# Optimization experiments

Measured on AMD Instinct MI355X. Metric: run time of the kernel, lower is better.

The kernel has to match this reference:

```python
import jax, jax.numpy as jnp
import numpy as np

HIDDEN = 4096
N_HEADS = 32
N_KV_HEADS = 8
HEAD_DIM = HIDDEN // N_HEADS  # 128
N_GROUPS = N_HEADS // N_KV_HEADS  # 4
ROPE_THETA = 10000.0
NEG_INF = -1e9


def fake_quant(x):
    """Symmetric per-tensor int8 fake quantization (quantize -> dequantize)."""
    scale = jnp.maximum(jnp.max(jnp.abs(x)) / 127.0, 1e-8)
    return jnp.clip(jnp.round(x / scale), -127.0, 127.0) * scale


def q_linear(x, W):
    # torch Linear: y = x @ W.T ; both operands fake-quantized (dequant-inline GEMM)
    return jnp.einsum('bsh,oh->bso', fake_quant(x), fake_quant(W))


def rope_cos_sin(position_ids, head_dim, dtype):
    inv_freq = 1.0 / (ROPE_THETA ** (jnp.arange(0, head_dim, 2, dtype=jnp.float32) / head_dim))
    freqs = position_ids.astype(jnp.float32)[..., None] * inv_freq  # [b, s, hd/2]
    emb = jnp.concatenate([freqs, freqs], axis=-1)                   # [b, s, hd]
    return jnp.cos(emb).astype(dtype), jnp.sin(emb).astype(dtype)


def rotate_half(x):
    x1, x2 = jnp.split(x, 2, axis=-1)
    return jnp.concatenate([-x2, x1], axis=-1)


def setup_inputs() -> dict:
    key = jax.random.key(0)
    ks = jax.random.split(key, 6)
    b, s = 2, 1024
    hidden_states = jax.random.normal(ks[0], (b, s, HIDDEN), dtype=jnp.float32)
    # additive causal mask [b, 1, q, kv]
    causal = jnp.where(jnp.tril(jnp.ones((s, s), dtype=bool)), 0.0, NEG_INF).astype(jnp.float32)
    attention_mask = jnp.broadcast_to(causal[None, None], (b, 1, s, s))
    position_ids = jnp.broadcast_to(jnp.arange(s, dtype=jnp.int64)[None, :], (b, s))
    winit = 1.0 / np.sqrt(HIDDEN)
    Wq = jax.random.normal(ks[1], (HIDDEN, HIDDEN), dtype=jnp.float32) * winit
    Wk = jax.random.normal(ks[2], (N_KV_HEADS * HEAD_DIM, HIDDEN), dtype=jnp.float32) * winit
    Wv = jax.random.normal(ks[3], (N_KV_HEADS * HEAD_DIM, HIDDEN), dtype=jnp.float32) * winit
    Wo = jax.random.normal(ks[4], (HIDDEN, HIDDEN), dtype=jnp.float32) * winit
    return {"hidden_states": hidden_states, "attention_mask": attention_mask,
            "position_ids": position_ids, "Wq": Wq, "Wk": Wk, "Wv": Wv, "Wo": Wo}


def reference(hidden_states, attention_mask, position_ids, Wq, Wk, Wv, Wo):
    b, s, _ = hidden_states.shape
    dtype = hidden_states.dtype

    # quantized QKV projections
    q = q_linear(hidden_states, Wq).reshape(b, s, N_HEADS, HEAD_DIM).transpose(0, 2, 1, 3)
    k = q_linear(hidden_states, Wk).reshape(b, s, N_KV_HEADS, HEAD_DIM).transpose(0, 2, 1, 3)
    v = q_linear(hidden_states, Wv).reshape(b, s, N_KV_HEADS, HEAD_DIM).transpose(0, 2, 1, 3)

    # RoPE
    cos, sin = rope_cos_sin(position_ids, HEAD_DIM, dtype)  # [b, s, hd]
    cos, sin = cos[:, None], sin[:, None]                   # broadcast over heads
    q = q * cos + rotate_half(q) * sin
    k = k * cos + rotate_half(k) * sin

    # GQA: repeat kv heads
    k = jnp.repeat(k, N_GROUPS, axis=1)  # [b, H, s, hd]
    v = jnp.repeat(v, N_GROUPS, axis=1)

    # quantized QK^T (per-tensor fake quant on both operands)
    attn = jnp.einsum('bhqd,bhkd->bhqk', fake_quant(q), fake_quant(k)) / jnp.sqrt(
        jnp.asarray(HEAD_DIM, dtype=jnp.float32)).astype(dtype)
    attn = attn + attention_mask
    attn = jax.nn.softmax(attn.astype(jnp.float32), axis=-1).astype(dtype)
    # attention_dropout = 0.0 (inference)

    # quantized AV matmul
    out = jnp.einsum('bhqk,bhkd->bhqd', fake_quant(attn), fake_quant(v))
    out = out.transpose(0, 2, 1, 3).reshape(b, s, HIDDEN)
    out = q_linear(out, Wo)
    return out
```

## Files before the change

kernel.cpp:

```cpp
#include <hip/hip_runtime.h>
#include <math.h>

#define B_ 2
#define S_ 1024
#define HID 4096
#define NH 32
#define NKV 8
#define HD 128
#define LOG2E 1.44269504088896340736f

typedef short s16x8 __attribute__((ext_vector_type(8)));
typedef float f32x4 __attribute__((ext_vector_type(4)));
typedef int i32x4 __attribute__((ext_vector_type(4)));
typedef unsigned short u16;
typedef unsigned uint4v __attribute__((ext_vector_type(4)));
typedef signed char s8;

__device__ __forceinline__ i32x4 mfma_i8(i32x4 a, i32x4 b, i32x4 c) {
  return __builtin_amdgcn_mfma_i32_16x16x64_i8(a, b, c, 0, 0, 0);
}
__device__ __forceinline__ float get_scale(const unsigned* sc, int slot) {
  return fmaxf(__uint_as_float(sc[slot]) / 127.0f, 1e-8f);
}
__device__ __forceinline__ int q127(float x, float s) {
  return (int)fminf(fmaxf(rintf(x / s), -127.f), 127.f);
}
__device__ __forceinline__ unsigned pack4(float4 v, float s) {
  return (q127(v.x, s) & 255) | ((q127(v.y, s) & 255) << 8) |
         ((q127(v.z, s) & 255) << 16) | ((q127(v.w, s) & 255) << 24);
}
__device__ __forceinline__ float max4(float4 v) {
  return fmaxf(fmaxf(fabsf(v.x), fabsf(v.y)), fmaxf(fabsf(v.z), fabsf(v.w)));
}
__device__ __forceinline__ void gload16(const void* g, void* l) {
  __builtin_amdgcn_global_load_lds(
      (const __attribute__((address_space(1))) unsigned*)g,
      (__attribute__((address_space(3))) unsigned*)l, 16, 0, 0);
}
__device__ __forceinline__ void atomic_absmax(unsigned* out, float m, int lane) {
  #pragma unroll
  for (int o = 32; o >= 1; o >>= 1) m = fmaxf(m, __shfl_xor(m, o));
  if (lane == 0) atomicMax(out, __float_as_uint(m));
}

#define SB_() __builtin_amdgcn_sched_barrier(0)
#define PBAR() do { SB_(); __builtin_amdgcn_s_barrier(); SB_(); } while (0)
#define VM6() do { SB_(); asm volatile("s_waitcnt vmcnt(6)" ::: "memory"); } while (0)
#define VM0() do { SB_(); asm volatile("s_waitcnt vmcnt(0)" ::: "memory"); } while (0)

__device__ __forceinline__ void tensor_pick(int blk, int& r, int& b0, int& nb) {
  if (blk < 342)       { r = 0; b0 = 0;    nb = 342; }
  else if (blk < 1024) { r = 1; b0 = 342;  nb = 682; }
  else if (blk < 1195) { r = 2; b0 = 1024; nb = 171; }
  else if (blk < 1366) { r = 3; b0 = 1195; nb = 171; }
  else                 { r = 4; b0 = 1366; nb = 682; }
}

__global__ void absmax5_k(const float4* __restrict__ p0, const float4* __restrict__ p1,
                          const float4* __restrict__ p2, const float4* __restrict__ p3,
                          const float4* __restrict__ p4, unsigned* __restrict__ sc) {
  int r, b0, nb;
  tensor_pick(blockIdx.x, r, b0, nb);
  const float4* x; int n4;
  if (r == 0)      { x = p0; n4 = B_ * S_ * HID / 4; }
  else if (r == 1) { x = p1; n4 = HID * HID / 4; }
  else if (r == 2) { x = p2; n4 = NKV * HD * HID / 4; }
  else if (r == 3) { x = p3; n4 = NKV * HD * HID / 4; }
  else             { x = p4; n4 = HID * HID / 4; }
  const int ng = n4 >> 2;
  const int stride = nb * 256;
  float m0 = 0.f, m1 = 0.f, m2 = 0.f, m3 = 0.f;
  for (int g = (blockIdx.x - b0) * 256 + threadIdx.x; g < ng; g += stride) {
    const float4* p = x + g * 4;
    float4 v0 = p[0], v1 = p[1], v2 = p[2], v3 = p[3];
    m0 = fmaxf(m0, max4(v0)); m1 = fmaxf(m1, max4(v1));
    m2 = fmaxf(m2, max4(v2)); m3 = fmaxf(m3, max4(v3));
  }
  float m = fmaxf(fmaxf(m0, m1), fmaxf(m2, m3));
  atomic_absmax(sc + r, m, threadIdx.x & 63);
}

__global__ void quant5_k(const float4* __restrict__ p0, const float4* __restrict__ p1,
                         const float4* __restrict__ p2, const float4* __restrict__ p3,
                         const float4* __restrict__ p4,
                         unsigned* __restrict__ y0, unsigned* __restrict__ y1,
                         unsigned* __restrict__ y2, unsigned* __restrict__ y3,
                         unsigned* __restrict__ y4, const unsigned* __restrict__ sc) {
  int r, b0, nb;
  tensor_pick(blockIdx.x, r, b0, nb);
  const float4* x; unsigned* y; int n4;
  if (r == 0)      { x = p0; y = y0; n4 = B_ * S_ * HID / 4; }
  else if (r == 1) { x = p1; y = y1; n4 = HID * HID / 4; }
  else if (r == 2) { x = p2; y = y2; n4 = NKV * HD * HID / 4; }
  else if (r == 3) { x = p3; y = y3; n4 = NKV * HD * HID / 4; }
  else             { x = p4; y = y4; n4 = HID * HID / 4; }
  float s = get_scale(sc, r);
  const int ng = n4 >> 2;
  const int stride = nb * 256;
  for (int g = (blockIdx.x - b0) * 256 + threadIdx.x; g < ng; g += stride) {
    const float4* p = x + g * 4;
    float4 v0 = p[0], v1 = p[1], v2 = p[2], v3 = p[3];
    uint4v o;
    o[0] = pack4(v0, s); o[1] = pack4(v1, s);
    o[2] = pack4(v2, s); o[3] = pack4(v3, s);
    *(uint4v*)(y + g * 4) = o;
  }
}

__global__ void quant_k(const float4* __restrict__ x, unsigned* __restrict__ y, int n4,
                        const unsigned* __restrict__ sc, int slot) {
  float s = get_scale(sc, slot);
  const int ng = n4 >> 2;
  int stride = gridDim.x * blockDim.x;
  for (int g = blockIdx.x * blockDim.x + threadIdx.x; g < ng; g += stride) {
    const float4* p = x + g * 4;
    float4 v0 = p[0], v1 = p[1], v2 = p[2], v3 = p[3];
    uint4v o;
    o[0] = pack4(v0, s); o[1] = pack4(v1, s);
    o[2] = pack4(v2, s); o[3] = pack4(v3, s);
    *(uint4v*)(y + g * 4) = o;
  }
}

__global__ void add_k(const float4* __restrict__ p0, const float4* __restrict__ p1,
                      float4* __restrict__ out, int n4) {
  const int ng = n4 >> 2;
  int stride = gridDim.x * blockDim.x;
  for (int g = blockIdx.x * blockDim.x + threadIdx.x; g < ng; g += stride) {
    const float4* a = p0 + g * 4;
    const float4* b = p1 + g * 4;
    float4 a0 = a[0], a1 = a[1], a2 = a[2], a3 = a[3];
    float4 b0 = b[0], b1 = b[1], b2 = b[2], b3 = b[3];
    float4* o = out + g * 4;
    o[0] = make_float4(a0.x + b0.x, a0.y + b0.y, a0.z + b0.z, a0.w + b0.w);
    o[1] = make_float4(a1.x + b1.x, a1.y + b1.y, a1.z + b1.z, a1.w + b1.w);
    o[2] = make_float4(a2.x + b2.x, a2.y + b2.y, a2.z + b2.z, a2.w + b2.w);
    o[3] = make_float4(a3.x + b3.x, a3.y + b3.y, a3.z + b3.z, a3.w + b3.w);
  }
}

__device__ __forceinline__ void rdA(const s8* slot, int wm, int lr, int lg,
                                    i32x4 af[4][2]) {
  #pragma unroll
  for (int mi = 0; mi < 4; ++mi) {
    int row = wm * 64 + mi * 16 + lr;
    const char* base = (const char*)slot + row * 128;
    int sw = (row & 7) << 4;
    #pragma unroll
    for (int ks = 0; ks < 2; ++ks)
      af[mi][ks] = *(const i32x4*)(base + ((ks * 64 + lg * 16) ^ sw));
  }
}
__device__ __forceinline__ void rdB(const s8* slot, int wn, int lr, int lg,
                                    i32x4 bf[2][2]) {
  #pragma unroll
  for (int ni = 0; ni < 2; ++ni) {
    int row = wn * 32 + ni * 16 + lr;
    const char* base = (const char*)slot + row * 128;
    int sw = (row & 7) << 4;
    #pragma unroll
    for (int ks = 0; ks < 2; ++ks)
      bf[ni][ks] = *(const i32x4*)(base + ((ks * 64 + lg * 16) ^ sw));
  }
}
template <int PM, int PN>
__device__ __forceinline__ void mfma_phase(i32x4 (&acc)[2][2][4][2],
                                           const i32x4 (&af)[4][2],
                                           const i32x4 (&bf)[2][2]) {
  __builtin_amdgcn_s_setprio(1);
  #pragma unroll
  for (int mi = 0; mi < 4; ++mi)
    #pragma unroll
    for (int ni = 0; ni < 2; ++ni)
      #pragma unroll
      for (int ks = 0; ks < 2; ++ks)
        acc[PM][PN][mi][ni] = mfma_i8(af[mi][ks], bf[ni][ks], acc[PM][PN][mi][ni]);
  __builtin_amdgcn_s_setprio(0);
}

__device__ void gemm256(const s8* __restrict__ A, const s8* __restrict__ Bm,
                        float* __restrict__ C, int Ncols, int m0, int n0,
                        int k0, int nkt, float scale, unsigned* omax, s8* S) {
  const int tid = threadIdx.x;
  const int wave = tid >> 6, lane = tid & 63;
  const int lr = lane & 15, lg = lane >> 4;
  const int wm = wave >> 2, wn = wave & 3;
  s8* SA00 = S;          s8* SA01 = S + 16384;
  s8* SB00 = S + 32768;  s8* SB01 = S + 49152;
  s8* SA10 = S + 65536;  s8* SA11 = S + 81920;
  s8* SB10 = S + 98304;  s8* SB11 = S + 114688;
  const int r0 = tid >> 3;
  const int ce = ((tid & 7) * 16) ^ ((r0 & 7) << 4);
  const s8* pa0 = A + (size_t)(m0 + r0) * HID + k0 + ce;
  const s8* pa1 = pa0 + (size_t)128 * HID;
  const s8* pb0 = Bm + (size_t)(n0 + r0) * HID + k0 + ce;
  const s8* pb1 = pb0 + (size_t)128 * HID;
  const int wdst = wave * 1024;
  i32x4 acc[2][2][4][2] = {};
  i32x4 af[4][2], bf[2][2];

  auto STG = [&](const s8* p, s8* slot, int tcol) {
    const s8* g = p + tcol * 128;
    gload16(g, slot + wdst);
    gload16(g + (size_t)64 * HID, slot + 8192 + wdst);
  };

  STG(pa0, SA00, 0); STG(pb0, SB00, 0); STG(pa1, SA01, 0); STG(pb1, SB01, 0);
  STG(pa0, SA10, 1); STG(pb1, SB11, 1); STG(pa1, SA11, 1);
  VM6(); PBAR();

  #pragma unroll 1
  for (int t = 0; t < nkt; t += 2) {
    const bool g2 = t + 2 < nkt, g3 = t + 3 < nkt;
    rdA(SA00, wm, lr, lg, af); rdB(SB00, wn, lr, lg, bf);
    STG(pb0, SB10, t + 1);
    PBAR(); mfma_phase<0, 0>(acc, af, bf); PBAR();
    rdB(SB01, wn, lr, lg, bf);
    if (g2) STG(pa0, SA00, t + 2);
    PBAR(); mfma_phase<0, 1>(acc, af, bf); PBAR();
    rdA(SA01, wm, lr, lg, af);
    if (g2) STG(pb1, SB01, t + 2);
    PBAR(); mfma_phase<1, 1>(acc, af, bf); PBAR();
    rdB(SB00, wn, lr, lg, bf);
    if (g2) STG(pa1, SA01, t + 2);
    PBAR(); mfma_phase<1, 0>(acc, af, bf);
    if (g2) { VM6(); } else { VM0(); }
    PBAR();
    rdA(SA10, wm, lr, lg, af); rdB(SB10, wn, lr, lg, bf);
    if (g2) STG(pb0, SB00, t + 2);
    PBAR(); mfma_phase<0, 0>(acc, af, bf); PBAR();
    rdB(SB11, wn, lr, lg, bf);
    if (g3) STG(pa0, SA10, t + 3);
    PBAR(); mfma_phase<0, 1>(acc, af, bf); PBAR();
    rdA(SA11, wm, lr, lg, af);
    if (g3) STG(pb1, SB11, t + 3);
    PBAR(); mfma_phase<1, 1>(acc, af, bf); PBAR();
    rdB(SB10, wn, lr, lg, bf);
    if (g3) STG(pa1, SA11, t + 3);
    PBAR(); mfma_phase<1, 0>(acc, af, bf); VM6(); PBAR();
  }

  float gm = 0.f;
  #pragma unroll
  for (int mh = 0; mh < 2; ++mh)
    #pragma unroll
    for (int nh = 0; nh < 2; ++nh)
      #pragma unroll
      for (int mi = 0; mi < 4; ++mi)
        #pragma unroll
        for (int ni = 0; ni < 2; ++ni) {
          size_t rbase = (size_t)(m0 + mh * 128 + wm * 64 + mi * 16 + lg * 4);
          int cb = n0 + nh * 128 + wn * 32 + ni * 16 + lr;
          #pragma unroll
          for (int r = 0; r < 4; ++r) {
            float v = (float)acc[mh][nh][mi][ni][r] * scale;
            gm = fmaxf(gm, fabsf(v));
            C[(rbase + r) * (size_t)Ncols + cb] = v;
          }
        }
  if (omax) atomic_absmax(omax, gm, lane);
}

__global__ __launch_bounds__(512, 1) void gemm_qkv8(
    const s8* __restrict__ Xq, const s8* __restrict__ Wqb,
    const s8* __restrict__ Wkb, const s8* __restrict__ Wvb,
    float* __restrict__ qf, float* __restrict__ kf, float* __restrict__ vf,
    const unsigned* __restrict__ sc, unsigned* __restrict__ vmax) {
  extern __shared__ __align__(16) s8 S[];
  int raw = blockIdx.x;
  int wg = (raw & 7) * 24 + (raw >> 3);
  int bx = wg & 7, by = wg >> 3;
  const s8* Bm; float* C; int Ncols, n0, sslot; unsigned* om = nullptr;
  if (by < 16)      { Bm = Wqb; C = qf; Ncols = HID;      n0 = by * 256;        sslot = 1; }
  else if (by < 20) { Bm = Wkb; C = kf; Ncols = NKV * HD; n0 = (by - 16) * 256; sslot = 2; }
  else              { Bm = Wvb; C = vf; Ncols = NKV * HD; n0 = (by - 20) * 256; sslot = 3; om = vmax; }
  float scale = get_scale(sc, 0) * get_scale(sc, sslot);
  gemm256(Xq, Bm, C, Ncols, bx * 256, n0, 0, 32, scale, om, S);
}

__global__ __launch_bounds__(512, 1) void gemm_o8(
    const s8* __restrict__ A, const s8* __restrict__ Bm,
    float* __restrict__ P0, float* __restrict__ P1,
    const unsigned* __restrict__ sc) {
  extern __shared__ __align__(16) s8 S[];
  int raw = blockIdx.x;
  int wg = (raw & 7) * 32 + (raw >> 3);
  int tile = wg >> 1, half = wg & 1;
  int by = tile & 15, bx = tile >> 4;
  float scale = get_scale(sc, 8) * get_scale(sc, 4);
  gemm256(A, Bm, half ? P1 : P0, HID, bx * 256, by * 256, half * 2048, 16,
          scale, nullptr, S);
}

__global__ void rope_tab_k(float2* __restrict__ tab) {
  int i = blockIdx.x * 256 + threadIdx.x;
  int pos = i >> 6, d = i & 63;
  float inv = exp2f((float)d * (-13.287712379549449f / 64.0f));
  float ang = (float)pos * inv;
  tab[i] = make_float2(cosf(ang), sinf(ang));
}

__global__ void rope2_k(float* __restrict__ qf, float* __restrict__ kf,
                        unsigned* __restrict__ sc, const float2* __restrict__ tab) {
  int reg = blockIdx.y;
  float* q = reg ? kf : qf;
  int nheads = reg ? NKV : NH;
  unsigned* om = sc + (reg ? 6 : 5);
  int total = B_ * S_ * nheads * 16;
  int stride = gridDim.x * blockDim.x;
  float m = 0.f;
  for (int i = blockIdx.x * blockDim.x + threadIdx.x; i < total; i += stride) {
    int g = i & 15;
    int h = (i >> 4) % nheads;
    int bs = i / (16 * nheads);
    int pos = bs & (S_ - 1);
    size_t base = ((size_t)bs * nheads + h) * HD + g * 4;
    float4 x1 = *(float4*)(q + base);
    float4 x2 = *(float4*)(q + base + 64);
    const float4* t = (const float4*)(tab + ((size_t)pos << 6) + g * 4);
    float4 t0 = t[0], t1 = t[1];
    float4 o1, o2;
    o1.x = x1.x * t0.x - x2.x * t0.y;  o2.x = x2.x * t0.x + x1.x * t0.y;
    o1.y = x1.y * t0.z - x2.y * t0.w;  o2.y = x2.y * t0.z + x1.y * t0.w;
    o1.z = x1.z * t1.x - x2.z * t1.y;  o2.z = x2.z * t1.x + x1.z * t1.y;
    o1.w = x1.w * t1.z - x2.w * t1.w;  o2.w = x2.w * t1.z + x1.w * t1.w;
    *(float4*)(q + base) = o1;
    *(float4*)(q + base + 64) = o2;
    m = fmaxf(m, fmaxf(max4(o1), max4(o2)));
  }
  atomic_absmax(om, m, threadIdx.x & 63);
}

__global__ void quantqk_k(const float4* __restrict__ qf, const float4* __restrict__ kf,
                          unsigned* __restrict__ qq, unsigned* __restrict__ kq,
                          const unsigned* __restrict__ sc) {
  int reg = blockIdx.y;
  const float4* x = reg ? kf : qf;
  unsigned* y = reg ? kq : qq;
  int n4 = reg ? (B_ * S_ * NKV * HD / 4) : (B_ * S_ * HID / 4);
  float s = get_scale(sc, reg ? 6 : 5);
  const int ng = n4 >> 2;
  int stride = gridDim.x * blockDim.x;
  for (int g = blockIdx.x * blockDim.x + threadIdx.x; g < ng; g += stride) {
    const float4* p = x + g * 4;
    float4 v0 = p[0], v1 = p[1], v2 = p[2], v3 = p[3];
    uint4v o;
    o[0] = pack4(v0, s); o[1] = pack4(v1, s);
    o[2] = pack4(v2, s); o[3] = pack4(v3, s);
    *(uint4v*)(y + g * 4) = o;
  }
}

__global__ __launch_bounds__(256) void vquant_t_k(const float* __restrict__ vf,
                                                  s8* __restrict__ vt,
                                                  const unsigned* __restrict__ sc) {
  __shared__ __align__(16) s8 Ls[64][132];
  float s = get_scale(sc, 7);
  int st = blockIdx.x & 15, kvh = (blockIdx.x >> 4) & 7, b = blockIdx.x >> 7;
  int s0 = st * 64;
  #pragma unroll
  for (int i = 0; i < 8; ++i) {
    int o = i * 256 + threadIdx.x;
    int sr = o >> 5, c4 = o & 31;
    float4 v = *(const float4*)(vf + ((size_t)(b * S_ + s0 + sr)) * (NKV * HD) +
                                kvh * HD + c4 * 4);
    *(unsigned*)(&Ls[sr][c4 * 4]) =
        (q127(v.x, s) & 255) | ((q127(v.y, s) & 255) << 8) |
        ((q127(v.z, s) & 255) << 16) | ((q127(v.w, s) & 255) << 24);
  }
  __syncthreads();
  s8* base = vt + (size_t)(b * NKV + kvh) * 131072 + st * 128;
  #pragma unroll
  for (int i = 0; i < 8; ++i) {
    int o = i * 256 + threadIdx.x;
    int j = o >> 5, half = (o >> 4) & 1, w = o & 15;
    int d = 2 * j + half;
    unsigned pk = (unsigned)(unsigned char)Ls[4 * w + 0][d] |
                  ((unsigned)(unsigned char)Ls[4 * w + 1][d] << 8) |
                  ((unsigned)(unsigned char)Ls[4 * w + 2][d] << 16) |
                  ((unsigned)(unsigned char)Ls[4 * w + 3][d] << 24);
    *(unsigned*)(base + (size_t)j * 2048 + half * 64 + ((w * 4) ^ ((j & 3) << 4))) = pk;
  }
}

__global__ __launch_bounds__(512) void attn_k(
    const s8* __restrict__ Q, const s8* __restrict__ Kq, const s8* __restrict__ Vt,
    float* __restrict__ O, const unsigned* __restrict__ sc, unsigned* __restrict__ omax) {
  __shared__ __align__(16) s8 Ks[2][64 * 128];
  __shared__ __align__(16) s8 Vs[2][64 * 128];
  __shared__ __align__(16) s8 Ps[128 * 64];
  const int tid = threadIdx.x;
  const int wave = tid >> 6, lane = tid & 63;
  const int lr = lane & 15, lg = lane >> 4;
  const int raw = blockIdx.x;
  const int xcd = raw & 7, j = raw >> 3;
  const int grp = xcd + 8 * (j >> 4);
  const int within = j & 15;
  const int b = grp >> 3, kvh = grp & 7;
  const int h = kvh * 4 + (within >> 2);
  const int qp = within & 3;
  const float sq = get_scale(sc, 5), sk = get_scale(sc, 6), sv = get_scale(sc, 7);
  const float c2 = sq * sk * 0.08838834764831845f * LOG2E;
  const float M0 = 32.0f;
  const int k_row = tid >> 3;
  const int k_cb = ((tid & 7) * 16) ^ ((k_row & 7) << 4);
  const s8* vbase = Vt + (size_t)(b * NKV + kvh) * 131072 +
                    (size_t)(tid >> 3) * 2048 + (tid & 7) * 16;
  float gmax = 0.f;

  auto stageK = [&](int buf, int kt) {
    gload16(Kq + (size_t)(b * S_ + kt * 64 + k_row) * (NKV * HD) + kvh * HD + k_cb,
            Ks[buf] + wave * 1024);
  };
  auto stageV = [&](int buf, int kt) {
    gload16(vbase + kt * 128, Vs[buf] + wave * 1024);
  };

  for (int pi = 0; pi < 2; ++pi) {
    const int qt = pi ? 7 - qp : qp;
    const int q0 = qt * 128;
    const int nkt = 2 * (qt + 1);
    const int qwmin = q0 + wave * 16;
    i32x4 aq[2];
    {
      const s8* qp_ = Q + (size_t)(b * S_ + q0 + wave * 16 + lr) * HID + h * HD + lg * 16;
      aq[0] = *(const i32x4*)(qp_);
      aq[1] = *(const i32x4*)(qp_ + 64);
    }
    float ll[4] = {0.f, 0.f, 0.f, 0.f};

    stageK(0, 0);
    __syncthreads();
    for (int kt = 0; kt < nkt; ++kt) {
      const int p = kt & 1;
      if (kt < nkt - 1) stageK(p ^ 1, kt + 1);
      i32x4 sacc[4] = {};
      __builtin_amdgcn_s_setprio(1);
      #pragma unroll
      for (int ks = 0; ks < 2; ++ks)
        #pragma unroll
        for (int n = 0; n < 4; ++n) {
          int row = n * 16 + lr;
          i32x4 bk = *(const i32x4*)((const char*)Ks[p] + row * 128 +
                                     ((ks * 64 + lg * 16) ^ ((row & 7) << 4)));
          sacc[n] = mfma_i8(aq[ks], bk, sacc[n]);
        }
      __builtin_amdgcn_s_setprio(0);
      if (kt * 64 + 63 <= qwmin) {
        #pragma unroll
        for (int r = 0; r < 4; ++r)
          #pragma unroll
          for (int n = 0; n < 4; ++n)
            ll[r] += exp2f(fmaf((float)sacc[n][r], c2, -M0));
      } else {
        #pragma unroll
        for (int r = 0; r < 4; ++r) {
          int qg = qwmin + lg * 4 + r;
          #pragma unroll
          for (int n = 0; n < 4; ++n) {
            int kg = kt * 64 + n * 16 + lr;
            float e = exp2f(fmaf((float)sacc[n][r], c2, -M0));
            ll[r] += (kg <= qg) ? e : 0.f;
          }
        }
      }
      __syncthreads();
    }
    float bias[4];
    #pragma unroll
    for (int r = 0; r < 4; ++r) {
      float l = ll[r];
      #pragma unroll
      for (int o = 8; o >= 1; o >>= 1) l += __shfl_xor(l, o);
      bias[r] = 6.9886846867721655f - __log2f(l) - M0;
    }

    i32x4 oacc[8] = {};
    stageK(0, 0); stageV(0, 0);
    __syncthreads();
    for (int kt = 0; kt < nkt; ++kt) {
      const int p = kt & 1;
      if (kt < nkt - 1) { stageK(p ^ 1, kt + 1); stageV(p ^ 1, kt + 1); }
      i32x4 sacc[4] = {};
      __builtin_amdgcn_s_setprio(1);
      #pragma unroll
      for (int ks = 0; ks < 2; ++ks)
        #pragma unroll
        for (int n = 0; n < 4; ++n) {
          int row = n * 16 + lr;
          i32x4 bk = *(const i32x4*)((const char*)Ks[p] + row * 128 +
                                     ((ks * 64 + lg * 16) ^ ((row & 7) << 4)));
          sacc[n] = mfma_i8(aq[ks], bk, sacc[n]);
        }
      __builtin_amdgcn_s_setprio(0);
      if (kt * 64 + 63 <= qwmin) {
        #pragma unroll
        for (int r = 0; r < 4; ++r) {
          int prow = wave * 16 + lg * 4 + r;
          s8* pr = Ps + prow * 64;
          #pragma unroll
          for (int n = 0; n < 4; ++n) {
            float p127 = rintf(exp2f(fmaf((float)sacc[n][r], c2, bias[r])));
            pr[((n * 16) ^ (lg << 4)) + lr] = (s8)(int)p127;
          }
        }
      } else {
        #pragma unroll
        for (int r = 0; r < 4; ++r) {
          int prow = wave * 16 + lg * 4 + r;
          int qg = qwmin + lg * 4 + r;
          s8* pr = Ps + prow * 64;
          #pragma unroll
          for (int n = 0; n < 4; ++n) {
            int kg = kt * 64 + n * 16 + lr;
            float a = fmaf((float)sacc[n][r], c2, bias[r]);
            float p127 = (kg <= qg) ? rintf(exp2f(a)) : 0.f;
            pr[((n * 16) ^ (lg << 4)) + lr] = (s8)(int)p127;
          }
        }
      }
      __builtin_amdgcn_s_setprio(1);
      {
        i32x4 ap = *(const i32x4*)(Ps + (wave * 16 + lr) * 64 +
                                   ((lg * 16) ^ (((lr >> 2) & 3) << 4)));
        #pragma unroll
        for (int n = 0; n < 8; ++n) {
          int jd = n * 8 + (lr >> 1);
          i32x4 bv = *(const i32x4*)((const char*)Vs[p] + jd * 128 + (lr & 1) * 64 +
                                     ((lg * 16) ^ ((jd & 3) << 4)));
          oacc[n] = mfma_i8(ap, bv, oacc[n]);
        }
      }
      __builtin_amdgcn_s_setprio(0);
      __syncthreads();
    }
    const float pvs = sv * (1.0f / 127.0f);
    #pragma unroll
    for (int n = 0; n < 8; ++n)
      #pragma unroll
      for (int r = 0; r < 4; ++r) {
        float v = (float)oacc[n][r] * pvs;
        gmax = fmaxf(gmax, fabsf(v));
        O[(size_t)(b * S_ + q0 + wave * 16 + lg * 4 + r) * HID + h * HD + n * 16 + lr] = v;
      }
  }
  atomic_absmax(omax, gmax, lane);
}

extern "C" void kernel_launch(void* const* d_in, const int* in_sizes, int n_in,
                              void* d_out, int out_size, void* d_ws, size_t ws_size,
                              hipStream_t stream) {
  const float* hs = (const float*)d_in[0];
  const float* Wq = (const float*)d_in[3];
  const float* Wk = (const float*)d_in[4];
  const float* Wv = (const float*)d_in[5];
  const float* Wo = (const float*)d_in[6];
  float* out = (float*)d_out;
  char* ws = (char*)d_ws;

  unsigned* sc = (unsigned*)ws;
  size_t off = 256;
  s8* Xq = (s8*)(ws + off); off += (size_t)B_ * S_ * HID;
  size_t wqb_off = off;
  s8* Wqb = (s8*)(ws + off); off += (size_t)HID * HID;
  s8* Wkb = (s8*)(ws + off); off += (size_t)NKV * HD * HID;
  s8* Wvb = (s8*)(ws + off); off += (size_t)NKV * HD * HID;
  s8* Wob = (s8*)(ws + off); off += (size_t)HID * HID;
  size_t qf_off = off;
  float* qf = (float*)(ws + off); off += (size_t)B_ * S_ * HID * 4;
  float* kf = (float*)(ws + off); off += (size_t)B_ * S_ * NKV * HD * 4;
  float* vf = (float*)(ws + off); off += (size_t)B_ * S_ * NKV * HD * 4;
  s8* qq = (s8*)(ws + off); off += (size_t)B_ * S_ * HID;
  s8* kq = (s8*)(ws + off); off += (size_t)B_ * S_ * NKV * HD;
  s8* vt = (s8*)(ws + off); off += (size_t)B_ * S_ * NKV * HD;
  float2* tab = (float2*)(ws + off); off += (size_t)S_ * 64 * 8;
  float* P1 = (float*)(ws + off); off += (size_t)B_ * S_ * HID * 4;
  float* attnf = (float*)(ws + qf_off);
  s8* attnq = (s8*)(ws + wqb_off);
  float* P0 = (float*)(ws + qf_off);

  hipFuncSetAttribute((const void*)gemm_qkv8,
                      hipFuncAttributeMaxDynamicSharedMemorySize, 131072);
  hipFuncSetAttribute((const void*)gemm_o8,
                      hipFuncAttributeMaxDynamicSharedMemorySize, 131072);

  hipMemsetAsync(sc, 0, 64, stream);

  dim3 blk(256);
  absmax5_k<<<2048, blk, 0, stream>>>(
      (const float4*)hs, (const float4*)Wq, (const float4*)Wk,
      (const float4*)Wv, (const float4*)Wo, sc);
  quant5_k<<<2048, blk, 0, stream>>>(
      (const float4*)hs, (const float4*)Wq, (const float4*)Wk,
      (const float4*)Wv, (const float4*)Wo,
      (unsigned*)Xq, (unsigned*)Wqb, (unsigned*)Wkb, (unsigned*)Wvb,
      (unsigned*)Wob, sc);
  rope_tab_k<<<256, blk, 0, stream>>>(tab);

  gemm_qkv8<<<192, 512, 131072, stream>>>(Xq, Wqb, Wkb, Wvb, qf, kf, vf, sc, sc + 7);

  rope2_k<<<dim3(512, 2), blk, 0, stream>>>(qf, kf, sc, tab);
  quantqk_k<<<dim3(512, 2), blk, 0, stream>>>((const float4*)qf, (const float4*)kf,
                                              (unsigned*)qq, (unsigned*)kq, sc);
  vquant_t_k<<<256, blk, 0, stream>>>(vf, vt, sc);

  attn_k<<<256, 512, 0, stream>>>(qq, kq, vt, attnf, sc, sc + 8);

  quant_k<<<2048, blk, 0, stream>>>((const float4*)attnf, (unsigned*)attnq,
                                    B_ * S_ * HID / 4, sc, 8);
  gemm_o8<<<256, 512, 131072, stream>>>(attnq, Wob, P0, P1, sc);
  add_k<<<2048, blk, 0, stream>>>((const float4*)P0, (const float4*)P1,
                                  (float4*)out, B_ * S_ * HID / 4);
}
```

Baseline: 446.7 us.

## Fuse RoPE into QKV GEMM epilogue and drop split-K in output GEMM

The QKV GEMM epilogue now stages each 128-column accumulator half in shared memory and applies RoPE in place, computing the q/k absmax directly. This removes the separate rope2_k pass over q and k. The output projection no longer splits K in two with partial buffers and an add kernel; it runs 128 full-K workgroups that write straight to the output. This saves the partial-buffer traffic and two launches, but the output GEMM now fills only half as many CUs, and the RoPE epilogue adds shared-memory round trips and extra barriers.

```diff
diff --git a/kernel.cpp b/kernel.cpp
--- a/kernel.cpp
+++ b/kernel.cpp
@@ -122,23 +122,6 @@
   }
 }
 
-__global__ void add_k(const float4* __restrict__ p0, const float4* __restrict__ p1,
-                      float4* __restrict__ out, int n4) {
-  const int ng = n4 >> 2;
-  int stride = gridDim.x * blockDim.x;
-  for (int g = blockIdx.x * blockDim.x + threadIdx.x; g < ng; g += stride) {
-    const float4* a = p0 + g * 4;
-    const float4* b = p1 + g * 4;
-    float4 a0 = a[0], a1 = a[1], a2 = a[2], a3 = a[3];
-    float4 b0 = b[0], b1 = b[1], b2 = b[2], b3 = b[3];
-    float4* o = out + g * 4;
-    o[0] = make_float4(a0.x + b0.x, a0.y + b0.y, a0.z + b0.z, a0.w + b0.w);
-    o[1] = make_float4(a1.x + b1.x, a1.y + b1.y, a1.z + b1.z, a1.w + b1.w);
-    o[2] = make_float4(a2.x + b2.x, a2.y + b2.y, a2.z + b2.z, a2.w + b2.w);
-    o[3] = make_float4(a3.x + b3.x, a3.y + b3.y, a3.z + b3.z, a3.w + b3.w);
-  }
-}
-
 __device__ __forceinline__ void rdA(const s8* slot, int wm, int lr, int lg,
                                     i32x4 af[4][2]) {
   #pragma unroll
@@ -180,7 +163,8 @@
 
 __device__ void gemm256(const s8* __restrict__ A, const s8* __restrict__ Bm,
                         float* __restrict__ C, int Ncols, int m0, int n0,
-                        int k0, int nkt, float scale, unsigned* omax, s8* S) {
+                        int k0, int nkt, float scale, unsigned* omax,
+                        const float2* __restrict__ tab, int doRope, s8* S) {
   const int tid = threadIdx.x;
   const int wave = tid >> 6, lane = tid & 63;
   const int lr = lane & 15, lg = lane >> 4;
@@ -241,23 +225,59 @@
   }
 
   float gm = 0.f;
-  #pragma unroll
-  for (int mh = 0; mh < 2; ++mh)
-    #pragma unroll
-    for (int nh = 0; nh < 2; ++nh)
-      #pragma unroll
-      for (int mi = 0; mi < 4; ++mi)
-        #pragma unroll
-        for (int ni = 0; ni < 2; ++ni) {
-          size_t rbase = (size_t)(m0 + mh * 128 + wm * 64 + mi * 16 + lg * 4);
-          int cb = n0 + nh * 128 + wn * 32 + ni * 16 + lr;
-          #pragma unroll
-          for (int r = 0; r < 4; ++r) {
-            float v = (float)acc[mh][nh][mi][ni][r] * scale;
-            gm = fmaxf(gm, fabsf(v));
-            C[(rbase + r) * (size_t)Ncols + cb] = v;
+  if (!doRope) {
+    #pragma unroll
+    for (int mh = 0; mh < 2; ++mh)
+      #pragma unroll
+      for (int nh = 0; nh < 2; ++nh)
+        #pragma unroll
+        for (int mi = 0; mi < 4; ++mi)
+          #pragma unroll
+          for (int ni = 0; ni < 2; ++ni) {
+            size_t rbase = (size_t)(m0 + mh * 128 + wm * 64 + mi * 16 + lg * 4);
+            int cb = n0 + nh * 128 + wn * 32 + ni * 16 + lr;
+            #pragma unroll
+            for (int r = 0; r < 4; ++r) {
+              float v = (float)acc[mh][nh][mi][ni][r] * scale;
+              gm = fmaxf(gm, fabsf(v));
+              C[(rbase + r) * (size_t)Ncols + cb] = v;
+            }
           }
-        }
+  } else {
+    __syncthreads();
+    float* Lf = (float*)S;
+    #pragma unroll
+    for (int mh = 0; mh < 2; ++mh)
+      #pragma unroll
+      for (int nh = 0; nh < 2; ++nh) {
+        #pragma unroll
+        for (int mi = 0; mi < 4; ++mi)
+          #pragma unroll
+          for (int ni = 0; ni < 2; ++ni)
+            #pragma unroll
+            for (int r = 0; r < 4; ++r)
+              Lf[(wm * 64 + mi * 16 + lg * 4 + r) * 128 + wn * 32 + ni * 16 + lr] =
+                  (float)acc[mh][nh][mi][ni][r] * scale;
+        __syncthreads();
+        #pragma unroll
+        for (int mi = 0; mi < 4; ++mi)
+          #pragma unroll
+          for (int ni = 0; ni < 2; ++ni)
+            #pragma unroll
+            for (int r = 0; r < 4; ++r) {
+              int rloc = wm * 64 + mi * 16 + lg * 4 + r;
+              int cloc = wn * 32 + ni * 16 + lr;
+              float v = Lf[rloc * 128 + cloc];
+              float w = Lf[rloc * 128 + (cloc ^ 64)];
+              int grow = m0 + mh * 128 + rloc;
+              float2 cs = tab[((grow & (S_ - 1)) << 6) + (cloc & 63)];
+              float o = (cloc < 64) ? v * cs.x - w * cs.y : v * cs.x + w * cs.y;
+              gm = fmaxf(gm, fabsf(o));
+              C[(size_t)grow * Ncols + (n0 + nh * 128 + cloc)] = o;
+            }
+        __syncthreads();
+      }
+  }
   if (omax) atomic_absmax(omax, gm, lane);
 }
 
@@ -265,31 +285,30 @@
     const s8* __restrict__ Xq, const s8* __restrict__ Wqb,
     const s8* __restrict__ Wkb, const s8* __restrict__ Wvb,
     float* __restrict__ qf, float* __restrict__ kf, float* __restrict__ vf,
-    const unsigned* __restrict__ sc, unsigned* __restrict__ vmax) {
+    const unsigned* __restrict__ sc, unsigned* __restrict__ scq,
+    const float2* __restrict__ tab) {
   extern __shared__ __align__(16) s8 S[];
   int raw = blockIdx.x;
   int wg = (raw & 7) * 24 + (raw >> 3);
   int bx = wg & 7, by = wg >> 3;
-  const s8* Bm; float* C; int Ncols, n0, sslot; unsigned* om = nullptr;
-  if (by < 16)      { Bm = Wqb; C = qf; Ncols = HID;      n0 = by * 256;        sslot = 1; }
-  else if (by < 20) { Bm = Wkb; C = kf; Ncols = NKV * HD; n0 = (by - 16) * 256; sslot = 2; }
-  else              { Bm = Wvb; C = vf; Ncols = NKV * HD; n0 = (by - 20) * 256; sslot = 3; om = vmax; }
+  const s8* Bm; float* C; int Ncols, n0, sslot, doRope; unsigned* om;
+  if (by < 16)      { Bm = Wqb; C = qf; Ncols = HID;      n0 = by * 256;        sslot = 1; doRope = 1; om = scq + 5; }
+  else if (by < 20) { Bm = Wkb; C = kf; Ncols = NKV * HD; n0 = (by - 16) * 256; sslot = 2; doRope = 1; om = scq + 6; }
+  else              { Bm = Wvb; C = vf; Ncols = NKV * HD; n0 = (by - 20) * 256; sslot = 3; doRope = 0; om = scq + 7; }
   float scale = get_scale(sc, 0) * get_scale(sc, sslot);
-  gemm256(Xq, Bm, C, Ncols, bx * 256, n0, 0, 32, scale, om, S);
+  gemm256(Xq, Bm, C, Ncols, bx * 256, n0, 0, 32, scale, om, tab, doRope, S);
 }
 
 __global__ __launch_bounds__(512, 1) void gemm_o8(
     const s8* __restrict__ A, const s8* __restrict__ Bm,
-    float* __restrict__ P0, float* __restrict__ P1,
-    const unsigned* __restrict__ sc) {
+    float* __restrict__ Cout, const unsigned* __restrict__ sc) {
   extern __shared__ __align__(16) s8 S[];
   int raw = blockIdx.x;
-  int wg = (raw & 7) * 32 + (raw >> 3);
-  int tile = wg >> 1, half = wg & 1;
-  int by = tile & 15, bx = tile >> 4;
+  int wg = (raw & 7) * 16 + (raw >> 3);
+  int bx = wg >> 4, by = wg & 15;
   float scale = get_scale(sc, 8) * get_scale(sc, 4);
-  gemm256(A, Bm, half ? P1 : P0, HID, bx * 256, by * 256, half * 2048, 16,
-          scale, nullptr, S);
+  gemm256(A, Bm, Cout, HID, bx * 256, by * 256, 0, 32, scale, nullptr,
+          nullptr, 0, S);
 }
 
 __global__ void rope_tab_k(float2* __restrict__ tab) {
@@ -298,37 +317,6 @@
   float inv = exp2f((float)d * (-13.287712379549449f / 64.0f));
   float ang = (float)pos * inv;
   tab[i] = make_float2(cosf(ang), sinf(ang));
-}
-
-__global__ void rope2_k(float* __restrict__ qf, float* __restrict__ kf,
-                        unsigned* __restrict__ sc, const float2* __restrict__ tab) {
-  int reg = blockIdx.y;
-  float* q = reg ? kf : qf;
-  int nheads = reg ? NKV : NH;
-  unsigned* om = sc + (reg ? 6 : 5);
-  int total = B_ * S_ * nheads * 16;
-  int stride = gridDim.x * blockDim.x;
-  float m = 0.f;
-  for (int i = blockIdx.x * blockDim.x + threadIdx.x; i < total; i += stride) {
-    int g = i & 15;
-    int h = (i >> 4) % nheads;
-    int bs = i / (16 * nheads);
-    int pos = bs & (S_ - 1);
-    size_t base = ((size_t)bs * nheads + h) * HD + g * 4;
-    float4 x1 = *(float4*)(q + base);
-    float4 x2 = *(float4*)(q + base + 64);
-    const float4* t = (const float4*)(tab + ((size_t)pos << 6) + g * 4);
-    float4 t0 = t[0], t1 = t[1];
-    float4 o1, o2;
-    o1.x = x1.x * t0.x - x2.x * t0.y;  o2.x = x2.x * t0.x + x1.x * t0.y;
-    o1.y = x1.y * t0.z - x2.y * t0.w;  o2.y = x2.y * t0.z + x1.y * t0.w;
-    o1.z = x1.z * t1.x - x2.z * t1.y;  o2.z = x2.z * t1.x + x1.z * t1.y;
-    o1.w = x1.w * t1.z - x2.w * t1.w;  o2.w = x2.w * t1.z + x1.w * t1.w;
-    *(float4*)(q + base) = o1;
-    *(float4*)(q + base + 64) = o2;
-    m = fmaxf(m, fmaxf(max4(o1), max4(o2)));
-  }
-  atomic_absmax(om, m, threadIdx.x & 63);
 }
 
 __global__ void quantqk_k(const float4* __restrict__ qf, const float4* __restrict__ kf,
@@ -574,10 +562,8 @@
   s8* kq = (s8*)(ws + off); off += (size_t)B_ * S_ * NKV * HD;
   s8* vt = (s8*)(ws + off); off += (size_t)B_ * S_ * NKV * HD;
   float2* tab = (float2*)(ws + off); off += (size_t)S_ * 64 * 8;
-  float* P1 = (float*)(ws + off); off += (size_t)B_ * S_ * HID * 4;
   float* attnf = (float*)(ws + qf_off);
   s8* attnq = (s8*)(ws + wqb_off);
-  float* P0 = (float*)(ws + qf_off);
 
   hipFuncSetAttribute((const void*)gemm_qkv8,
                       hipFuncAttributeMaxDynamicSharedMemorySize, 131072);
@@ -597,9 +583,9 @@
       (unsigned*)Wob, sc);
   rope_tab_k<<<256, blk, 0, stream>>>(tab);
 
-  gemm_qkv8<<<192, 512, 131072, stream>>>(Xq, Wqb, Wkb, Wvb, qf, kf, vf, sc, sc + 7);
-
-  rope2_k<<<dim3(512, 2), blk, 0, stream>>>(qf, kf, sc, tab);
+  gemm_qkv8<<<192, 512, 131072, stream>>>(Xq, Wqb, Wkb, Wvb, qf, kf, vf,
+                                          sc, sc, tab);
+
   quantqk_k<<<dim3(512, 2), blk, 0, stream>>>((const float4*)qf, (const float4*)kf,
                                               (unsigned*)qq, (unsigned*)kq, sc);
   vquant_t_k<<<256, blk, 0, stream>>>(vf, vt, sc);
@@ -608,7 +594,5 @@
 
   quant_k<<<2048, blk, 0, stream>>>((const float4*)attnf, (unsigned*)attnq,
                                     B_ * S_ * HID / 4, sc, 8);
-  gemm_o8<<<256, 512, 131072, stream>>>(attnq, Wob, P0, P1, sc);
-  add_k<<<2048, blk, 0, stream>>>((const float4*)P0, (const float4*)P1,
-                                  (float4*)out, B_ * S_ * HID / 4);
-}
+  gemm_o8<<<128, 512, 131072, stream>>>(attnq, Wob, out, sc);
+}
```

Result: slower. 462.1 us (+3.4%).
